# Optimization experiments

Measured on AMD Instinct MI355X. Metric: run time of the kernel, lower is better.

## Reference

```python
import jax, jax.numpy as jnp
import numpy as np

B, T, D, E, H, K = 4, 4096, 1024, 8, 512, 2  # batch, seq, n_embed, num_experts, bottleneck, top_k


def setup_inputs() -> dict:
    key = jax.random.key(0)
    ks = jax.random.split(key, 8)
    s = 0.02  # param scale (original zero-inits adapters; random used for a meaningful baseline)
    return {
        "x": jax.random.normal(ks[0], (B, T, D), jnp.float32),
        "Wr": (jax.random.normal(ks[1], (D, E), jnp.float32) * s),
        "br": jnp.zeros((E,), jnp.float32),
        "Wn": (jax.random.normal(ks[2], (D, E), jnp.float32) * s),
        "bn": jnp.zeros((E,), jnp.float32),
        "Wd": (jax.random.normal(ks[3], (E, D, H), jnp.float32) * s),
        "bd": jnp.zeros((E, H), jnp.float32),
        "Wu": (jax.random.normal(ks[4], (E, H, D), jnp.float32) * s),
        "bu": jnp.zeros((E, D), jnp.float32),
        "noise": jax.random.normal(ks[5], (B, T, E), jnp.float32),
        "top_k": K,
    }


def reference(x, Wr, br, Wn, bn, Wd, bd, Wu, bu, noise, top_k):
    # --- NoisyTopkRouter ---
    logits = x @ Wr + br                                   # [B,T,E]
    noise_logits = x @ Wn + bn                             # [B,T,E]
    noisy = logits + noise * jax.nn.softplus(noise_logits)  # randn * softplus(noise_logits)
    _, idx = jax.lax.top_k(noisy, top_k)                   # [B,T,K]
    # mask of selected experts; where(mask, noisy, -inf) == scatter(top_k_logits into -inf)
    mask = jax.nn.one_hot(idx, noisy.shape[-1], dtype=jnp.bool_).any(axis=-2)  # [B,T,E]
    sparse = jnp.where(mask, noisy, -jnp.inf)
    gates = jax.nn.softmax(sparse, axis=-1)                # zeros for unselected experts

    # --- Experts (dense grouped form; gate==0 exactly kills unselected experts incl. biases) ---
    down = jnp.einsum('btd,edh->bteh', x, Wd) + bd         # [B,T,E,H]
    hidden = jax.nn.gelu(down, approximate=False)          # torch GELU is exact (erf)
    up = jnp.einsum('bteh,ehd->bted', hidden, Wu) + bu     # [B,T,E,D]
    return jnp.einsum('bted,bte->btd', up, gates)          # gate-weighted combine
```

## Files before the change

kernel.cpp:

```cpp
#include <hip/hip_runtime.h>
#include <hip/hip_bf16.h>
#include <hip/hip_fp16.h>
#include <math.h>

#define DD   1024
#define EE   8
#define HH   512
#define NTOK 16384
#define NG   16
#define MAXMT 24

typedef __attribute__((ext_vector_type(8))) short short8;
typedef __attribute__((ext_vector_type(4))) float floatx4;

__device__ __forceinline__ ushort f2bfu(float f) {
    __hip_bfloat16 h = __float2bfloat16(f);
    return *reinterpret_cast<ushort*>(&h);
}

__device__ __forceinline__ void glds16(const void* g, void* l) {
    __builtin_amdgcn_global_load_lds(
        (const __attribute__((address_space(1))) unsigned int*)g,
        (__attribute__((address_space(3))) unsigned int*)l, 16, 0, 0);
}

__global__ void zero_k(int* __restrict__ cnt) {
    if (blockIdx.x == 0 && threadIdx.x < 256) cnt[threadIdx.x] = 0;
}

__global__ __launch_bounds__(256) void cvtx_k(const float* __restrict__ x, ushort* __restrict__ xb) {
    const size_t i = ((size_t)blockIdx.x * 256 + threadIdx.x) * 8;
    const float4 a = *(const float4*)(x + i);
    const float4 b = *(const float4*)(x + i + 4);
    ushort o[8];
    o[0]=f2bfu(a.x); o[1]=f2bfu(a.y); o[2]=f2bfu(a.z); o[3]=f2bfu(a.w);
    o[4]=f2bfu(b.x); o[5]=f2bfu(b.y); o[6]=f2bfu(b.z); o[7]=f2bfu(b.w);
    *(uint4*)(xb + i) = *(uint4*)o;
}

__global__ __launch_bounds__(256) void trans_k(const float* __restrict__ src, ushort* __restrict__ dst,
                                               const int R, const int C) {
    const int e = blockIdx.z, r0 = blockIdx.y * 64, c0 = blockIdx.x * 64;
    __shared__ float t[64][65];
    const int tid = threadIdx.x;
    const int cseg = (tid & 15) * 4, rr = tid >> 4;
#pragma unroll
    for (int j = 0; j < 4; ++j) {
        const int r = rr + j * 16;
        const float4 v = *(const float4*)(src + ((size_t)e * R + r0 + r) * C + c0 + cseg);
        t[r][cseg] = v.x; t[r][cseg+1] = v.y; t[r][cseg+2] = v.z; t[r][cseg+3] = v.w;
    }
    __syncthreads();
    const int rseg = (tid & 15) * 4;
#pragma unroll
    for (int j = 0; j < 4; ++j) {
        const int crow = (tid >> 4) + j * 16;
        ushort o[4];
#pragma unroll
        for (int q = 0; q < 4; ++q) o[q] = f2bfu(t[rseg + q][crow]);
        *(uint2*)(dst + ((size_t)e * C + c0 + crow) * R + r0 + rseg) = *(uint2*)o;
    }
}

__global__ __launch_bounds__(256) void router_k(
    const float* __restrict__ x, const float* __restrict__ Wr, const float* __restrict__ br,
    const float* __restrict__ Wn, const float* __restrict__ bn, const float* __restrict__ noise,
    int* __restrict__ cnt, unsigned* __restrict__ entries)
{
    const int wave = threadIdx.x >> 6;
    const int lane = threadIdx.x & 63;
    const int t = blockIdx.x * 4 + wave;

    float accr[EE], accn[EE];
#pragma unroll
    for (int e = 0; e < EE; ++e) { accr[e] = 0.f; accn[e] = 0.f; }

    const float* xr = x + (size_t)t * DD;
#pragma unroll 4
    for (int it = 0; it < DD / 64; ++it) {
        const int d = it * 64 + lane;
        const float xv = xr[d];
        float wr[8], wn[8];
        *(float4*)&wr[0] = *(const float4*)(Wr + (size_t)d * EE);
        *(float4*)&wr[4] = *(const float4*)(Wr + (size_t)d * EE + 4);
        *(float4*)&wn[0] = *(const float4*)(Wn + (size_t)d * EE);
        *(float4*)&wn[4] = *(const float4*)(Wn + (size_t)d * EE + 4);
#pragma unroll
        for (int e = 0; e < EE; ++e) {
            accr[e] = fmaf(xv, wr[e], accr[e]);
            accn[e] = fmaf(xv, wn[e], accn[e]);
        }
    }
#pragma unroll
    for (int off = 32; off > 0; off >>= 1) {
#pragma unroll
        for (int e = 0; e < EE; ++e) {
            accr[e] += __shfl_xor(accr[e], off);
            accn[e] += __shfl_xor(accn[e], off);
        }
    }
    if (lane == 0) {
        float noisy[EE];
#pragma unroll
        for (int e = 0; e < EE; ++e) {
            const float lg = accr[e] + br[e];
            const float nl = accn[e] + bn[e];
            const float sp = fmaxf(nl, 0.f) + log1pf(expf(-fabsf(nl)));
            noisy[e] = lg + noise[(size_t)t * EE + e] * sp;
        }
        int i0 = 0;
#pragma unroll
        for (int e = 1; e < EE; ++e) if (noisy[e] > noisy[i0]) i0 = e;
        int i1 = (i0 == 0) ? 1 : 0;
#pragma unroll
        for (int e = 0; e < EE; ++e) if (e != i0 && noisy[e] > noisy[i1]) i1 = e;
        const float ex = expf(noisy[i1] - noisy[i0]);
        const float g0 = 1.f / (1.f + ex);
        const float g1 = ex / (1.f + ex);
        __half h0 = __float2half_rn(g0), h1 = __float2half_rn(g1);
        const unsigned u0 = (unsigned)t | ((unsigned)*reinterpret_cast<ushort*>(&h0) << 16);
        const unsigned u1 = (unsigned)t | ((unsigned)*reinterpret_cast<ushort*>(&h1) << 16);
        const int ga = i0 * 2 + 0, gb = i1 * 2 + 1;
        int p0 = atomicAdd(&cnt[ga * 16], 1);
        entries[ga * NTOK + p0] = u0;
        int p1 = atomicAdd(&cnt[gb * 16], 1);
        entries[gb * NTOK + p1] = u1;
    }
}

__global__ void offsets_k(const int* __restrict__ cnt, int* __restrict__ off) {
    if (threadIdx.x == 0 && blockIdx.x == 0) {
        int s = 0;
        for (int g = 0; g < NG; ++g) { off[g] = s; s += cnt[g * 16]; }
    }
}


__global__ __launch_bounds__(256) void down_k(
    const ushort* __restrict__ xb, const ushort* __restrict__ WdT, const float* __restrict__ bd,
    const int* __restrict__ cnt, const int* __restrict__ off,
    const unsigned* __restrict__ entries, ushort* __restrict__ hid)
{
    const int g = blockIdx.z, e = g >> 1;
    const int n_g = cnt[g * 16];
    const int tm = blockIdx.y;
    if (tm * 128 >= n_g) return;
    const int n0 = blockIdx.x * 128;

    __shared__ __align__(16) ushort As[128 * 32];
    __shared__ __align__(16) ushort Bs[128 * 32];
    __shared__ unsigned ecache[128];

    const int tid = threadIdx.x, lane = tid & 63, w = tid >> 6;
    const int wm = w >> 1, wn = w & 1;
    const int fr = lane & 15, fq = lane >> 4;

    if (tid < 128) {
        const int ridx = min(tm * 128 + tid, n_g - 1);
        ecache[tid] = entries[g * NTOK + ridx];
    }
    __syncthreads();

    const int u0 = w * 64 + lane;
    const int rowA0 = u0 >> 2, rowA1 = rowA0 + 64, seg = u0 & 3;
    const ushort* gA0 = xb + (size_t)(ecache[rowA0] & 0xFFFFu) * DD + seg * 8;
    const ushort* gA1 = xb + (size_t)(ecache[rowA1] & 0xFFFFu) * DD + seg * 8;
    const ushort* WTe = WdT + (size_t)e * HH * DD;
    const ushort* gB0 = WTe + (size_t)(n0 + rowA0) * DD + seg * 8;
    const ushort* gB1 = WTe + (size_t)(n0 + rowA1) * DD + seg * 8;
    char* lA0 = (char*)As + (size_t)(w * 64) * 16;
    char* lA1 = (char*)As + (size_t)(256 + w * 64) * 16;
    char* lB0 = (char*)Bs + (size_t)(w * 64) * 16;
    char* lB1 = (char*)Bs + (size_t)(256 + w * 64) * 16;

    floatx4 acc[4][4];
#pragma unroll
    for (int i = 0; i < 4; ++i)
#pragma unroll
        for (int j = 0; j < 4; ++j) acc[i][j] = (floatx4){0.f, 0.f, 0.f, 0.f};

    for (int k0 = 0; k0 < DD; k0 += 32) {
        __syncthreads();
        glds16(gA0 + k0, lA0);
        glds16(gA1 + k0, lA1);
        glds16(gB0 + k0, lB0);
        glds16(gB1 + k0, lB1);
        __syncthreads();
        short8 a[4], b[4];
#pragma unroll
        for (int mt = 0; mt < 4; ++mt)
            a[mt] = *(const short8*)&As[(wm * 64 + mt * 16 + fr) * 32 + fq * 8];
#pragma unroll
        for (int nt = 0; nt < 4; ++nt)
            b[nt] = *(const short8*)&Bs[(wn * 64 + nt * 16 + fr) * 32 + fq * 8];
#pragma unroll
        for (int mt = 0; mt < 4; ++mt)
#pragma unroll
            for (int nt = 0; nt < 4; ++nt)
                acc[mt][nt] = __builtin_amdgcn_mfma_f32_16x16x32_bf16(a[mt], b[nt], acc[mt][nt], 0, 0, 0);
    }

    const int hbase = off[g] + tm * 128;
#pragma unroll
    for (int nt = 0; nt < 4; ++nt) {
        const int n = n0 + wn * 64 + nt * 16 + fr;
        const float bias = bd[e * HH + n];
#pragma unroll
        for (int mt = 0; mt < 4; ++mt)
#pragma unroll
            for (int i = 0; i < 4; ++i) {
                const int rl = wm * 64 + mt * 16 + fq * 4 + i;
                if (tm * 128 + rl < n_g) {
                    const float v = acc[mt][nt][i] + bias;
                    const float ge = 0.5f * v * (1.f + erff(v * 0.7071067811865475f));
                    hid[(size_t)(hbase + rl) * HH + n] = f2bfu(ge);
                }
            }
    }
}

__global__ __launch_bounds__(256) void up_k(
    const ushort* __restrict__ hid, const ushort* __restrict__ WuT, const float* __restrict__ bu,
    const int* __restrict__ cnt, const int* __restrict__ off,
    const unsigned* __restrict__ entries, float* __restrict__ out, const int s)
{
    const int e = blockIdx.z, g = e * 2 + s;
    const int n_g = cnt[g * 16];
    const int tm = blockIdx.y;
    if (tm * 128 >= n_g) return;
    const int n0 = blockIdx.x * 128;

    __shared__ __align__(16) ushort As[128 * 32];
    __shared__ __align__(16) ushort Bs[128 * 32];
    __shared__ unsigned ecache[128];

    const int tid = threadIdx.x, lane = tid & 63, w = tid >> 6;
    const int wm = w >> 1, wn = w & 1;
    const int fr = lane & 15, fq = lane >> 4;

    if (tid < 128) {
        const int ridx = min(tm * 128 + tid, n_g - 1);
        ecache[tid] = entries[g * NTOK + ridx];
    }
    __syncthreads();

    const int u0 = w * 64 + lane;
    const int rowA0 = u0 >> 2, rowA1 = rowA0 + 64, seg = u0 & 3;
    const int ar0 = min(tm * 128 + rowA0, n_g - 1);
    const int ar1 = min(tm * 128 + rowA1, n_g - 1);
    const ushort* gA0 = hid + (size_t)(off[g] + ar0) * HH + seg * 8;
    const ushort* gA1 = hid + (size_t)(off[g] + ar1) * HH + seg * 8;
    const ushort* WTe = WuT + (size_t)e * DD * HH;
    const ushort* gB0 = WTe + (size_t)(n0 + rowA0) * HH + seg * 8;
    const ushort* gB1 = WTe + (size_t)(n0 + rowA1) * HH + seg * 8;
    char* lA0 = (char*)As + (size_t)(w * 64) * 16;
    char* lA1 = (char*)As + (size_t)(256 + w * 64) * 16;
    char* lB0 = (char*)Bs + (size_t)(w * 64) * 16;
    char* lB1 = (char*)Bs + (size_t)(256 + w * 64) * 16;

    floatx4 acc[4][4];
#pragma unroll
    for (int i = 0; i < 4; ++i)
#pragma unroll
        for (int j = 0; j < 4; ++j) acc[i][j] = (floatx4){0.f, 0.f, 0.f, 0.f};

    for (int k0 = 0; k0 < HH; k0 += 32) {
        __syncthreads();
        glds16(gA0 + k0, lA0);
        glds16(gA1 + k0, lA1);
        glds16(gB0 + k0, lB0);
        glds16(gB1 + k0, lB1);
        __syncthreads();
        short8 a[4], b[4];
#pragma unroll
        for (int mt = 0; mt < 4; ++mt)
            a[mt] = *(const short8*)&As[(wm * 64 + mt * 16 + fr) * 32 + fq * 8];
#pragma unroll
        for (int nt = 0; nt < 4; ++nt)
            b[nt] = *(const short8*)&Bs[(wn * 64 + nt * 16 + fr) * 32 + fq * 8];
#pragma unroll
        for (int mt = 0; mt < 4; ++mt)
#pragma unroll
            for (int nt = 0; nt < 4; ++nt)
                acc[mt][nt] = __builtin_amdgcn_mfma_f32_16x16x32_bf16(a[mt], b[nt], acc[mt][nt], 0, 0, 0);
    }

#pragma unroll
    for (int nt = 0; nt < 4; ++nt) {
        const int n = n0 + wn * 64 + nt * 16 + fr;
        const float bias = bu[e * DD + n];
#pragma unroll
        for (int mt = 0; mt < 4; ++mt)
#pragma unroll
            for (int i = 0; i < 4; ++i) {
                const int rl = wm * 64 + mt * 16 + fq * 4 + i;
                if (tm * 128 + rl < n_g) {
                    const unsigned en = ecache[rl];
                    const int tok = (int)(en & 0xFFFFu);
                    ushort hb = (ushort)(en >> 16);
                    const float gate = __half2float(*reinterpret_cast<__half*>(&hb));
                    const float v = (acc[mt][nt][i] + bias) * gate;
                    float* op = out + (size_t)tok * DD + n;
                    if (s == 0) *op = v;
                    else        *op += v;
                }
            }
    }
}

extern "C" void kernel_launch(void* const* d_in, const int* in_sizes, int n_in,
                              void* d_out, int out_size, void* d_ws, size_t ws_size,
                              hipStream_t stream)
{
    const float* x     = (const float*)d_in[0];
    const float* Wr    = (const float*)d_in[1];
    const float* br    = (const float*)d_in[2];
    const float* Wn    = (const float*)d_in[3];
    const float* bn    = (const float*)d_in[4];
    const float* Wd    = (const float*)d_in[5];
    const float* bd    = (const float*)d_in[6];
    const float* Wu    = (const float*)d_in[7];
    const float* bu    = (const float*)d_in[8];
    const float* noise = (const float*)d_in[9];

    char* ws = (char*)d_ws;
    int*      cnt     = (int*)(ws + 0);
    int*      off     = (int*)(ws + 1024);
    unsigned* entries = (unsigned*)(ws + 2048);
    ushort*   xb      = (ushort*)(ws + 1050624);
    ushort*   WdT     = (ushort*)(ws + 34605056);
    ushort*   WuT     = (ushort*)(ws + 42993664);
    ushort*   hid     = (ushort*)(ws + 51382272);

    zero_k<<<1, 256, 0, stream>>>(cnt);
    cvtx_k<<<(NTOK * DD) / (256 * 8), 256, 0, stream>>>(x, xb);
    trans_k<<<dim3(HH / 64, DD / 64, EE), 256, 0, stream>>>(Wd, WdT, DD, HH);
    trans_k<<<dim3(DD / 64, HH / 64, EE), 256, 0, stream>>>(Wu, WuT, HH, DD);
    router_k<<<NTOK / 4, 256, 0, stream>>>(x, Wr, br, Wn, bn, noise, cnt, entries);
    offsets_k<<<1, 64, 0, stream>>>(cnt, off);
    down_k<<<dim3(HH / 128, MAXMT, NG), 256, 0, stream>>>(xb, WdT, bd, cnt, off, entries, hid);
    up_k<<<dim3(DD / 128, MAXMT, EE), 256, 0, stream>>>(hid, WuT, bu, cnt, off, entries, (float*)d_out, 0);
    up_k<<<dim3(DD / 128, MAXMT, EE), 256, 0, stream>>>(hid, WuT, bu, cnt, off, entries, (float*)d_out, 1);
}
```

Measured before the change: 458.4 us.

## Fuse bf16 cast into router, widen K tile with XOR swizzle, merge up passes via atomics

Removes the separate x-to-bf16 conversion kernel by writing bf16 x from the router while it reads x. Doubles the K tile of both grouped GEMMs to 64 and applies an XOR swizzle to the LDS layout, which halves barrier count and reduces bank conflicts. The two up-projection launches become one launch over all groups that accumulates into a memset-zeroed output with float atomics. The cost is an extra memset, atomic traffic, and a summation order that is no longer fixed.

```diff
diff --git a/kernel.cpp b/kernel.cpp
--- a/kernel.cpp
+++ b/kernel.cpp
@@ -28,16 +28,6 @@
     if (blockIdx.x == 0 && threadIdx.x < 256) cnt[threadIdx.x] = 0;
 }
 
-__global__ __launch_bounds__(256) void cvtx_k(const float* __restrict__ x, ushort* __restrict__ xb) {
-    const size_t i = ((size_t)blockIdx.x * 256 + threadIdx.x) * 8;
-    const float4 a = *(const float4*)(x + i);
-    const float4 b = *(const float4*)(x + i + 4);
-    ushort o[8];
-    o[0]=f2bfu(a.x); o[1]=f2bfu(a.y); o[2]=f2bfu(a.z); o[3]=f2bfu(a.w);
-    o[4]=f2bfu(b.x); o[5]=f2bfu(b.y); o[6]=f2bfu(b.z); o[7]=f2bfu(b.w);
-    *(uint4*)(xb + i) = *(uint4*)o;
-}
-
 __global__ __launch_bounds__(256) void trans_k(const float* __restrict__ src, ushort* __restrict__ dst,
                                                const int R, const int C) {
     const int e = blockIdx.z, r0 = blockIdx.y * 64, c0 = blockIdx.x * 64;
@@ -65,7 +55,7 @@
 __global__ __launch_bounds__(256) void router_k(
     const float* __restrict__ x, const float* __restrict__ Wr, const float* __restrict__ br,
     const float* __restrict__ Wn, const float* __restrict__ bn, const float* __restrict__ noise,
-    int* __restrict__ cnt, unsigned* __restrict__ entries)
+    int* __restrict__ cnt, unsigned* __restrict__ entries, ushort* __restrict__ xb)
 {
     const int wave = threadIdx.x >> 6;
     const int lane = threadIdx.x & 63;
@@ -76,10 +66,12 @@
     for (int e = 0; e < EE; ++e) { accr[e] = 0.f; accn[e] = 0.f; }
 
     const float* xr = x + (size_t)t * DD;
+    ushort* xbr = xb + (size_t)t * DD;
 #pragma unroll 4
     for (int it = 0; it < DD / 64; ++it) {
         const int d = it * 64 + lane;
         const float xv = xr[d];
+        xbr[d] = f2bfu(xv);
         float wr[8], wn[8];
         *(float4*)&wr[0] = *(const float4*)(Wr + (size_t)d * EE);
         *(float4*)&wr[4] = *(const float4*)(Wr + (size_t)d * EE + 4);
@@ -147,8 +139,8 @@
     if (tm * 128 >= n_g) return;
     const int n0 = blockIdx.x * 128;
 
-    __shared__ __align__(16) ushort As[128 * 32];
-    __shared__ __align__(16) ushort Bs[128 * 32];
+    __shared__ __align__(16) ushort As[128 * 64];
+    __shared__ __align__(16) ushort Bs[128 * 64];
     __shared__ unsigned ecache[128];
 
     const int tid = threadIdx.x, lane = tid & 63, w = tid >> 6;
@@ -161,17 +153,20 @@
     }
     __syncthreads();
 
-    const int u0 = w * 64 + lane;
-    const int rowA0 = u0 >> 2, rowA1 = rowA0 + 64, seg = u0 & 3;
-    const ushort* gA0 = xb + (size_t)(ecache[rowA0] & 0xFFFFu) * DD + seg * 8;
-    const ushort* gA1 = xb + (size_t)(ecache[rowA1] & 0xFFFFu) * DD + seg * 8;
+    const int lr = lane >> 3, seg = lane & 7;
+    const int slog = seg ^ lr;
+    const ushort* gA[4]; const ushort* gB[4];
+    char* lA[4]; char* lB[4];
     const ushort* WTe = WdT + (size_t)e * HH * DD;
-    const ushort* gB0 = WTe + (size_t)(n0 + rowA0) * DD + seg * 8;
-    const ushort* gB1 = WTe + (size_t)(n0 + rowA1) * DD + seg * 8;
-    char* lA0 = (char*)As + (size_t)(w * 64) * 16;
-    char* lA1 = (char*)As + (size_t)(256 + w * 64) * 16;
-    char* lB0 = (char*)Bs + (size_t)(w * 64) * 16;
-    char* lB1 = (char*)Bs + (size_t)(256 + w * 64) * 16;
+#pragma unroll
+    for (int j = 0; j < 4; ++j) {
+        const int row = w * 32 + j * 8 + lr;
+        const int tok = (int)(ecache[row] & 0xFFFFu);
+        gA[j] = xb + (size_t)tok * DD + slog * 8;
+        gB[j] = WTe + (size_t)(n0 + row) * DD + slog * 8;
+        lA[j] = (char*)As + (size_t)(w * 256 + j * 64) * 16;
+        lB[j] = (char*)Bs + (size_t)(w * 256 + j * 64) * 16;
+    }
 
     floatx4 acc[4][4];
 #pragma unroll
@@ -179,25 +174,33 @@
 #pragma unroll
         for (int j = 0; j < 4; ++j) acc[i][j] = (floatx4){0.f, 0.f, 0.f, 0.f};
 
-    for (int k0 = 0; k0 < DD; k0 += 32) {
+    const int axr = wm * 64 + fr;
+    const int bxr = wn * 64 + fr;
+
+    for (int k0 = 0; k0 < DD; k0 += 64) {
         __syncthreads();
-        glds16(gA0 + k0, lA0);
-        glds16(gA1 + k0, lA1);
-        glds16(gB0 + k0, lB0);
-        glds16(gB1 + k0, lB1);
+#pragma unroll
+        for (int j = 0; j < 4; ++j) { glds16(gA[j] + k0, lA[j]); glds16(gB[j] + k0, lB[j]); }
         __syncthreads();
-        short8 a[4], b[4];
-#pragma unroll
-        for (int mt = 0; mt < 4; ++mt)
-            a[mt] = *(const short8*)&As[(wm * 64 + mt * 16 + fr) * 32 + fq * 8];
-#pragma unroll
-        for (int nt = 0; nt < 4; ++nt)
-            b[nt] = *(const short8*)&Bs[(wn * 64 + nt * 16 + fr) * 32 + fq * 8];
-#pragma unroll
-        for (int mt = 0; mt < 4; ++mt)
-#pragma unroll
-            for (int nt = 0; nt < 4; ++nt)
-                acc[mt][nt] = __builtin_amdgcn_mfma_f32_16x16x32_bf16(a[mt], b[nt], acc[mt][nt], 0, 0, 0);
+#pragma unroll
+        for (int kh = 0; kh < 2; ++kh) {
+            short8 a[4], b[4];
+#pragma unroll
+            for (int mt = 0; mt < 4; ++mt) {
+                const int r = axr + mt * 16;
+                a[mt] = *(const short8*)&As[r * 64 + ((kh * 4 + fq) ^ (r & 7)) * 8];
+            }
+#pragma unroll
+            for (int nt = 0; nt < 4; ++nt) {
+                const int r = bxr + nt * 16;
+                b[nt] = *(const short8*)&Bs[r * 64 + ((kh * 4 + fq) ^ (r & 7)) * 8];
+            }
+#pragma unroll
+            for (int mt = 0; mt < 4; ++mt)
+#pragma unroll
+                for (int nt = 0; nt < 4; ++nt)
+                    acc[mt][nt] = __builtin_amdgcn_mfma_f32_16x16x32_bf16(a[mt], b[nt], acc[mt][nt], 0, 0, 0);
+        }
     }
 
     const int hbase = off[g] + tm * 128;
@@ -222,16 +225,16 @@
 __global__ __launch_bounds__(256) void up_k(
     const ushort* __restrict__ hid, const ushort* __restrict__ WuT, const float* __restrict__ bu,
     const int* __restrict__ cnt, const int* __restrict__ off,
-    const unsigned* __restrict__ entries, float* __restrict__ out, const int s)
+    const unsigned* __restrict__ entries, float* __restrict__ out)
 {
-    const int e = blockIdx.z, g = e * 2 + s;
+    const int g = blockIdx.z, e = g >> 1;
     const int n_g = cnt[g * 16];
     const int tm = blockIdx.y;
     if (tm * 128 >= n_g) return;
     const int n0 = blockIdx.x * 128;
 
-    __shared__ __align__(16) ushort As[128 * 32];
-    __shared__ __align__(16) ushort Bs[128 * 32];
+    __shared__ __align__(16) ushort As[128 * 64];
+    __shared__ __align__(16) ushort Bs[128 * 64];
     __shared__ unsigned ecache[128];
 
     const int tid = threadIdx.x, lane = tid & 63, w = tid >> 6;
@@ -244,19 +247,21 @@
     }
     __syncthreads();
 
-    const int u0 = w * 64 + lane;
-    const int rowA0 = u0 >> 2, rowA1 = rowA0 + 64, seg = u0 & 3;
-    const int ar0 = min(tm * 128 + rowA0, n_g - 1);
-    const int ar1 = min(tm * 128 + rowA1, n_g - 1);
-    const ushort* gA0 = hid + (size_t)(off[g] + ar0) * HH + seg * 8;
-    const ushort* gA1 = hid + (size_t)(off[g] + ar1) * HH + seg * 8;
+    const int lr = lane >> 3, seg = lane & 7;
+    const int slog = seg ^ lr;
+    const ushort* gA[4]; const ushort* gB[4];
+    char* lA[4]; char* lB[4];
     const ushort* WTe = WuT + (size_t)e * DD * HH;
-    const ushort* gB0 = WTe + (size_t)(n0 + rowA0) * HH + seg * 8;
-    const ushort* gB1 = WTe + (size_t)(n0 + rowA1) * HH + seg * 8;
-    char* lA0 = (char*)As + (size_t)(w * 64) * 16;
-    char* lA1 = (char*)As + (size_t)(256 + w * 64) * 16;
-    char* lB0 = (char*)Bs + (size_t)(w * 64) * 16;
-    char* lB1 = (char*)Bs + (size_t)(256 + w * 64) * 16;
+    const int hbase = off[g];
+#pragma unroll
+    for (int j = 0; j < 4; ++j) {
+        const int row = w * 32 + j * 8 + lr;
+        const int ar = min(tm * 128 + row, n_g - 1);
+        gA[j] = hid + (size_t)(hbase + ar) * HH + slog * 8;
+        gB[j] = WTe + (size_t)(n0 + row) * HH + slog * 8;
+        lA[j] = (char*)As + (size_t)(w * 256 + j * 64) * 16;
+        lB[j] = (char*)Bs + (size_t)(w * 256 + j * 64) * 16;
+    }
 
     floatx4 acc[4][4];
 #pragma unroll
@@ -264,25 +269,33 @@
 #pragma unroll
         for (int j = 0; j < 4; ++j) acc[i][j] = (floatx4){0.f, 0.f, 0.f, 0.f};
 
-    for (int k0 = 0; k0 < HH; k0 += 32) {
+    const int axr = wm * 64 + fr;
+    const int bxr = wn * 64 + fr;
+
+    for (int k0 = 0; k0 < HH; k0 += 64) {
         __syncthreads();
-        glds16(gA0 + k0, lA0);
-        glds16(gA1 + k0, lA1);
-        glds16(gB0 + k0, lB0);
-        glds16(gB1 + k0, lB1);
+#pragma unroll
+        for (int j = 0; j < 4; ++j) { glds16(gA[j] + k0, lA[j]); glds16(gB[j] + k0, lB[j]); }
         __syncthreads();
-        short8 a[4], b[4];
-#pragma unroll
-        for (int mt = 0; mt < 4; ++mt)
-            a[mt] = *(const short8*)&As[(wm * 64 + mt * 16 + fr) * 32 + fq * 8];
-#pragma unroll
-        for (int nt = 0; nt < 4; ++nt)
-            b[nt] = *(const short8*)&Bs[(wn * 64 + nt * 16 + fr) * 32 + fq * 8];
-#pragma unroll
-        for (int mt = 0; mt < 4; ++mt)
-#pragma unroll
-            for (int nt = 0; nt < 4; ++nt)
-                acc[mt][nt] = __builtin_amdgcn_mfma_f32_16x16x32_bf16(a[mt], b[nt], acc[mt][nt], 0, 0, 0);
+#pragma unroll
+        for (int kh = 0; kh < 2; ++kh) {
+            short8 a[4], b[4];
+#pragma unroll
+            for (int mt = 0; mt < 4; ++mt) {
+                const int r = axr + mt * 16;
+                a[mt] = *(const short8*)&As[r * 64 + ((kh * 4 + fq) ^ (r & 7)) * 8];
+            }
+#pragma unroll
+            for (int nt = 0; nt < 4; ++nt) {
+                const int r = bxr + nt * 16;
+                b[nt] = *(const short8*)&Bs[r * 64 + ((kh * 4 + fq) ^ (r & 7)) * 8];
+            }
+#pragma unroll
+            for (int mt = 0; mt < 4; ++mt)
+#pragma unroll
+                for (int nt = 0; nt < 4; ++nt)
+                    acc[mt][nt] = __builtin_amdgcn_mfma_f32_16x16x32_bf16(a[mt], b[nt], acc[mt][nt], 0, 0, 0);
+        }
     }
 
 #pragma unroll
@@ -299,10 +312,7 @@
                     const int tok = (int)(en & 0xFFFFu);
                     ushort hb = (ushort)(en >> 16);
                     const float gate = __half2float(*reinterpret_cast<__half*>(&hb));
-                    const float v = (acc[mt][nt][i] + bias) * gate;
-                    float* op = out + (size_t)tok * DD + n;
-                    if (s == 0) *op = v;
-                    else        *op += v;
+                    unsafeAtomicAdd(out + (size_t)tok * DD + n, (acc[mt][nt][i] + bias) * gate);
                 }
             }
     }
@@ -332,13 +342,12 @@
     ushort*   WuT     = (ushort*)(ws + 42993664);
     ushort*   hid     = (ushort*)(ws + 51382272);
 
+    hipMemsetAsync(d_out, 0, (size_t)NTOK * DD * sizeof(float), stream);
     zero_k<<<1, 256, 0, stream>>>(cnt);
-    cvtx_k<<<(NTOK * DD) / (256 * 8), 256, 0, stream>>>(x, xb);
     trans_k<<<dim3(HH / 64, DD / 64, EE), 256, 0, stream>>>(Wd, WdT, DD, HH);
     trans_k<<<dim3(DD / 64, HH / 64, EE), 256, 0, stream>>>(Wu, WuT, HH, DD);
-    router_k<<<NTOK / 4, 256, 0, stream>>>(x, Wr, br, Wn, bn, noise, cnt, entries);
+    router_k<<<NTOK / 4, 256, 0, stream>>>(x, Wr, br, Wn, bn, noise, cnt, entries, xb);
     offsets_k<<<1, 64, 0, stream>>>(cnt, off);
     down_k<<<dim3(HH / 128, MAXMT, NG), 256, 0, stream>>>(xb, WdT, bd, cnt, off, entries, hid);
-    up_k<<<dim3(DD / 128, MAXMT, EE), 256, 0, stream>>>(hid, WuT, bu, cnt, off, entries, (float*)d_out, 0);
-    up_k<<<dim3(DD / 128, MAXMT, EE), 256, 0, stream>>>(hid, WuT, bu, cnt, off, entries, (float*)d_out, 1);
-}
+    up_k<<<dim3(DD / 128, MAXMT, NG), 256, 0, stream>>>(hid, WuT, bu, cnt, off, entries, (float*)d_out);
+}
```

Result: slower. 497.4 us (+8.5%).
